# Performance work log

Measured on AMD Instinct MI355X. Metric: run time of the kernel, lower is better.

## Reference

```python
import jax, jax.numpy as jnp
import numpy as np

N = 200000   # nodes
E = 4000000  # edges
D = 32       # hidden dim (forced equal to edge-embed dim 32)
G = 512      # graphs in batch
OUT = 64     # conv5 output dim
BN_EPS = 1e-5


def _bn(h, g, b):
    # BatchNorm1d, training mode (fresh model): biased batch stats over node dim
    mu = jnp.mean(h, axis=0)
    var = jnp.var(h, axis=0)
    return g * (h - mu) * jax.lax.rsqrt(var + BN_EPS) + b


def _gine(h, src, dst, e, W1, b1, g, be, W2, b2, final_relu):
    # GINEConv (eps=0): out = MLP(x + sum_j ReLU(x_j + edge_attr))
    msg = jax.nn.relu(h[src] + e)                              # [E, D]
    agg = jax.ops.segment_sum(msg, dst, num_segments=h.shape[0])
    z = h + agg
    z = jax.nn.relu(_bn(z @ W1 + b1, g, be)) @ W2 + b2
    return jax.nn.relu(z) if final_relu else z


def setup_inputs() -> dict:
    key = jax.random.key(0)
    ks = jax.random.split(key, 16)
    xav = lambda k, shp: jax.random.uniform(k, shp, jnp.float32, -1.0, 1.0) * np.sqrt(6.0 / (shp[-2] + shp[-1]))
    x = jax.random.normal(ks[0], (N, D), jnp.float32)
    edge_index = jax.random.randint(ks[1], (2, E), 0, N, dtype=jnp.int32)
    edge_type = jax.random.randint(ks[2], (E,), 0, 2, dtype=jnp.int32)
    batch = jnp.sort(jax.random.randint(ks[3], (N,), 0, G, dtype=jnp.int32))
    emb = xav(ks[4], (2, D))  # xavier-initialized edge-type embedding
    # convs 1-4: Linear(D,D), BN(D), ReLU, Linear(D,D), ReLU  -> stacked [4,...]
    W1s = xav(ks[5], (4, D, D)); b1s = jnp.zeros((4, D))
    g1s = jnp.ones((4, D)); be1s = jnp.zeros((4, D))
    W2s = xav(ks[6], (4, D, D)); b2s = jnp.zeros((4, D))
    # conv 5: Linear(D,D), BN(D), ReLU, Linear(D,OUT)  (no final ReLU)
    w15 = xav(ks[7], (D, D)); b15 = jnp.zeros((D,))
    g5 = jnp.ones((D,)); be5 = jnp.zeros((D,))
    w25 = xav(ks[8], (D, OUT)); b25 = jnp.zeros((OUT,))
    return dict(x=x, edge_index=edge_index, edge_type=edge_type, batch=batch,
                emb=emb, W1s=W1s, b1s=b1s, g1s=g1s, be1s=be1s, W2s=W2s, b2s=b2s,
                w15=w15, b15=b15, g5=g5, be5=be5, w25=w25, b25=b25)


def reference(x, edge_index, edge_type, batch, emb, W1s, b1s, g1s, be1s, W2s, b2s,
              w15, b15, g5, be5, w25, b25):
    src, dst = edge_index[0], edge_index[1]
    e = emb[edge_type]                                          # [E, D]
    h = x
    for i in range(4):
        h = _gine(h, src, dst, e, W1s[i], b1s[i], g1s[i], be1s[i], W2s[i], b2s[i], True)
    h = _gine(h, src, dst, e, w15, b15, g5, be5, w25, b25, False)  # [N, OUT]
    mx = jax.ops.segment_max(h, batch, num_segments=G)
    cnt = jax.ops.segment_sum(jnp.ones((h.shape[0], 1), h.dtype), batch, num_segments=G)
    mn = jax.ops.segment_sum(h, batch, num_segments=G) / jnp.maximum(cnt, 1.0)
    return jnp.concatenate([mx, mn], axis=1)                    # [G, 2*OUT]
```

## Files before the change

kernel.cpp:

```cpp
#include <hip/hip_runtime.h>

#define NBLKA 2048

__device__ __forceinline__ unsigned encf(float x) {
    unsigned u = __float_as_uint(x);
    return (u & 0x80000000u) ? ~u : (u | 0x80000000u);
}
__device__ __forceinline__ float decf(unsigned u) {
    u = (u & 0x80000000u) ? (u & 0x7FFFFFFFu) : ~u;
    return __uint_as_float(u);
}
__device__ __forceinline__ unsigned bf16rne(float f) {
    unsigned u = __float_as_uint(f);
    return (u + 0x7FFFu + ((u >> 16) & 1u)) >> 16;
}


__global__ __launch_bounds__(256) void passA_k(const int* __restrict__ dst, int E,
                                               int* __restrict__ cntMat, int bshift,
                                               int nblk, int nb2) {
    __shared__ int hist[512];
    hist[threadIdx.x] = 0; hist[threadIdx.x + 256] = 0;
    __syncthreads();
    int base = blockIdx.x * 4096;
#pragma unroll
    for (int r = 0; r < 16; r++) {
        int i = base + threadIdx.x + r * 256;
        if (i < E) atomicAdd(&hist[dst[i] >> bshift], 1);
    }
    __syncthreads();
    for (int bk = threadIdx.x; bk < nb2; bk += 256)
        cntMat[bk * nblk + blockIdx.x] = hist[bk];
}

__global__ void scanA_k(int* __restrict__ data, int total, int* __restrict__ chunkTot) {
    __shared__ int sd[256];
    int tid = threadIdx.x;
    int base = blockIdx.x * 2048 + tid * 8;
    int v[8]; int s = 0;
#pragma unroll
    for (int r = 0; r < 8; r++) {
        int idx = base + r;
        int x = (idx < total) ? data[idx] : 0;
        s += x; v[r] = s;
    }
    sd[tid] = s; __syncthreads();
    for (int off = 1; off < 256; off <<= 1) {
        int x = (tid >= off) ? sd[tid - off] : 0;
        __syncthreads();
        sd[tid] += x;
        __syncthreads();
    }
    int prev = (tid > 0) ? sd[tid - 1] : 0;
#pragma unroll
    for (int r = 0; r < 8; r++) {
        int idx = base + r;
        if (idx < total) data[idx] = v[r] + prev;
    }
    if (tid == 255) chunkTot[blockIdx.x] = sd[255];
}

__global__ void scanB_k(const int* __restrict__ chunkTot, int nchunk, int* __restrict__ chunkOff) {
    __shared__ int sd[256];
    int tid = threadIdx.x;
    int v = (tid < nchunk) ? chunkTot[tid] : 0;
    sd[tid] = v; __syncthreads();
    for (int off = 1; off < 256; off <<= 1) {
        int x = (tid >= off) ? sd[tid - off] : 0;
        __syncthreads();
        sd[tid] += x;
        __syncthreads();
    }
    if (tid < nchunk) chunkOff[tid] = sd[tid] - v;
}

__global__ void scanC2_k(int* __restrict__ data, int total, const int* __restrict__ chunkOff) {
    int off = chunkOff[blockIdx.x];
    int base = blockIdx.x * 2048 + threadIdx.x * 8;
#pragma unroll
    for (int r = 0; r < 8; r++) {
        int idx = base + r;
        if (idx < total) data[idx] += off;
    }
}

__global__ __launch_bounds__(256) void passB_k(const int* __restrict__ ei,
                                               const int* __restrict__ ety, int E,
                                               const int* __restrict__ cntScan,
                                               unsigned* __restrict__ binned,
                                               int bshift, int sBits, int nblk, int nb2) {
    __shared__ unsigned stage[4096];
    __shared__ unsigned short bkid[4096];
    __shared__ int hist[512], sd[256], cursor[512], rebase[512];
    int tid = threadIdx.x;
    int base = blockIdx.x * 4096;
    hist[tid] = 0; hist[tid + 256] = 0;
    __syncthreads();

    unsigned ent[16];
    int bk[16];
    int lowmask = (1 << bshift) - 1;
    int dshift = sBits + 1;
#pragma unroll
    for (int r = 0; r < 16; r++) {
        int i = base + tid + r * 256;
        if (i < E) {
            int s = ei[i];
            int d = ei[E + i];
            int t = ety[i];
            ent[r] = ((unsigned)(d & lowmask) << dshift) | ((unsigned)t << sBits) | (unsigned)s;
            bk[r] = d >> bshift;
            atomicAdd(&hist[bk[r]], 1);
        } else bk[r] = -1;
    }
    __syncthreads();

    int v0 = hist[2 * tid], v1 = hist[2 * tid + 1];
    int sum2 = v0 + v1;
    sd[tid] = sum2; __syncthreads();
    for (int off = 1; off < 256; off <<= 1) {
        int x = (tid >= off) ? sd[tid - off] : 0;
        __syncthreads();
        sd[tid] += x;
        __syncthreads();
    }
    int exclPair = sd[tid] - sum2;
    __syncthreads();
    cursor[2 * tid] = exclPair;
    cursor[2 * tid + 1] = exclPair + v0;
    int b0 = 2 * tid, b1 = 2 * tid + 1;
    rebase[b0] = (b0 < nb2 && v0 > 0) ? (cntScan[b0 * nblk + blockIdx.x] - v0) - exclPair : 0;
    rebase[b1] = (b1 < nb2 && v1 > 0) ? (cntScan[b1 * nblk + blockIdx.x] - v1) - (exclPair + v0) : 0;
    __syncthreads();

#pragma unroll
    for (int r = 0; r < 16; r++) {
        if (bk[r] >= 0) {
            int p = atomicAdd(&cursor[bk[r]], 1);
            stage[p] = ent[r];
            bkid[p] = (unsigned short)bk[r];
        }
    }
    __syncthreads();

    int cnt = E - base; if (cnt > 4096) cnt = 4096;
    for (int i = tid; i < cnt; i += 256)
        binned[rebase[bkid[i]] + i] = stage[i];
}

__global__ __launch_bounds__(256) void passC_k(const unsigned* __restrict__ binned,
                                               const int* __restrict__ cntScan,
                                               int nblk, int* __restrict__ rowptr,
                                               unsigned* __restrict__ sorted,
                                               int N, int E, int bshift, int sBits,
                                               int nb2) {
    __shared__ int hist[512], cursor[512], sd[256];
    int tid = threadIdx.x;
    int b = blockIdx.x;
    int s = (b == 0) ? 0 : cntScan[b * nblk - 1];
    int e = cntScan[(b + 1) * nblk - 1];
    int nodeBase = b << bshift;
    int dshift = sBits + 1;

    hist[tid] = 0; hist[tid + 256] = 0;
    __syncthreads();
    for (int i = s + tid; i < e; i += 256)
        atomicAdd(&hist[(int)(binned[i] >> dshift)], 1);
    __syncthreads();

    int v0 = hist[2 * tid], v1 = hist[2 * tid + 1];
    int sum2 = v0 + v1;
    sd[tid] = sum2; __syncthreads();
    for (int off = 1; off < 256; off <<= 1) {
        int x = (tid >= off) ? sd[tid - off] : 0;
        __syncthreads();
        sd[tid] += x;
        __syncthreads();
    }
    int exclPair = sd[tid] - sum2;
    __syncthreads();
    cursor[2 * tid] = exclPair;
    cursor[2 * tid + 1] = exclPair + v0;
    int n0 = nodeBase + 2 * tid, n1 = nodeBase + 2 * tid + 1;
    if (n0 < N) rowptr[n0] = s + exclPair;
    if (n1 < N) rowptr[n1] = s + exclPair + v0;
    __syncthreads();

    for (int i = s + tid; i < e; i += 256) {
        unsigned en = binned[i];
        int ln = (int)(en >> dshift);
        int p = atomicAdd(&cursor[ln], 1);
        sorted[s + p] = en;
    }
    if (b == nb2 - 1 && tid == 0) rowptr[N] = E;
}

__global__ void initpool_k(unsigned* __restrict__ maxb, float* __restrict__ sumb, int n) {
    int i = blockIdx.x * blockDim.x + threadIdx.x;
    if (i < n) { maxb[i] = 0x007FFFFFu; sumb[i] = 0.f; }
}

__global__ void copyx_k(const float* __restrict__ x, unsigned* __restrict__ P,
                        unsigned* __restrict__ Q, int N) {
    int i = blockIdx.x * 256 + threadIdx.x;
    int tot = N * 16;
    if (i < tot) {
        float2 v = ((const float2*)x)[i];
        P[i] = bf16rne(v.x) | (bf16rne(v.y) << 16);
    }
    if (i < 16) {
        unsigned sp = bf16rne(-1e30f) | (bf16rne(-1e30f) << 16);
        P[tot + i] = sp;
        Q[tot + i] = sp;
    }
}

__global__ __launch_bounds__(256) void layerA_k(
    const unsigned* __restrict__ hin, const int* __restrict__ rowptr,
    const unsigned* __restrict__ sorted, const float* __restrict__ emb,
    const float* __restrict__ W1, const float* __restrict__ b1,
    float* __restrict__ tout, float* __restrict__ partial, int Nn, int sBits,
    unsigned sentw)
{
    float2* tout2 = (float2*)tout;
    int tid = threadIdx.x;
    int gl = tid & 31;
    int c = gl & 15;
    int slot = gl >> 4;
    int grp = tid >> 5;
    unsigned smask = (1u << sBits) - 1u;

    float2 w1c[16];
#pragma unroll
    for (int kk = 0; kk < 16; kk++)
        w1c[kk] = *(const float2*)&W1[(16 * slot + kk) * 32 + 2 * c];
    float2 b1p = *(const float2*)&b1[2 * c];
    float2 e0p = *(const float2*)&emb[2 * c];
    float2 e1p = *(const float2*)&emb[32 + 2 * c];

    __shared__ float zl[8][32];
    __shared__ float ls[8][32], lq[8][32];

    float2 bsum = {0.f, 0.f}, bsq = {0.f, 0.f};

    int gid0 = (blockIdx.x * 256 + tid) >> 5;
    int nG = (gridDim.x * 256) >> 5;

    for (int n = gid0; n < Nn; n += nG) {
        int es = rowptr[n], ee = rowptr[n + 1];
        float accx = 0.f, accy = 0.f;
        for (int e0 = es; e0 < ee; e0 += 32) {
            int idx = e0 + gl;
            unsigned pv = (idx < ee) ? sorted[idx] : sentw;
#pragma unroll
            for (int kk = 0; kk < 16; kk++) {
                unsigned p = (unsigned)__shfl((int)pv, kk, 16);
                unsigned s = p & smask;
                unsigned w = hin[s * 16u + (unsigned)c];
                float hx = __uint_as_float(w << 16);
                float hy = __uint_as_float(w & 0xFFFF0000u);
                bool t1 = ((p >> sBits) & 1u) != 0u;
                float evx = t1 ? e1p.x : e0p.x;
                float evy = t1 ? e1p.y : e0p.y;
                accx += fmaxf(hx + evx, 0.f);
                accy += fmaxf(hy + evy, 0.f);
            }
        }
        accx += __shfl_xor(accx, 16);
        accy += __shfl_xor(accy, 16);
        unsigned wn = hin[(unsigned)n * 16u + (unsigned)c];
        accx += __uint_as_float(wn << 16);
        accy += __uint_as_float(wn & 0xFFFF0000u);

        if (slot == 0) { zl[grp][2 * c] = accx; zl[grp][2 * c + 1] = accy; }
        float tx = 0.f, ty = 0.f;
#pragma unroll
        for (int kk = 0; kk < 16; kk++) {
            float zk = zl[grp][16 * slot + kk];
            tx = fmaf(zk, w1c[kk].x, tx);
            ty = fmaf(zk, w1c[kk].y, ty);
        }
        tx += __shfl_xor(tx, 16);
        ty += __shfl_xor(ty, 16);
        tx += b1p.x; ty += b1p.y;
        if (slot == 0) { float2 tp; tp.x = tx; tp.y = ty; tout2[(unsigned)n * 16u + (unsigned)c] = tp; }
        bsum.x += tx; bsum.y += ty;
        bsq.x = fmaf(tx, tx, bsq.x);
        bsq.y = fmaf(ty, ty, bsq.y);
    }

    if (slot == 0) {
        ls[grp][2 * c] = bsum.x; ls[grp][2 * c + 1] = bsum.y;
        lq[grp][2 * c] = bsq.x;  lq[grp][2 * c + 1] = bsq.y;
    }
    __syncthreads();
    if (tid < 32) {
        float s = 0.f, q = 0.f;
#pragma unroll
        for (int r = 0; r < 8; r++) { s += ls[r][tid]; q += lq[r][tid]; }
        partial[blockIdx.x * 64 + tid] = s;
        partial[blockIdx.x * 64 + 32 + tid] = q;
    }
}

__global__ __launch_bounds__(256) void bnred1_k(const float* __restrict__ partial,
                                                float* __restrict__ partial2) {
    __shared__ float sd[4][64];
    int tid = threadIdx.x;
    int c = tid & 63, q = tid >> 6;
    int rowBase = blockIdx.x * 32 + q * 8;
    float s = 0.f;
#pragma unroll
    for (int r = 0; r < 8; r++) s += partial[(rowBase + r) * 64 + c];
    sd[q][c] = s;
    __syncthreads();
    if (q == 0) partial2[blockIdx.x * 64 + c] = sd[0][c] + sd[1][c] + sd[2][c] + sd[3][c];
}

__global__ __launch_bounds__(256) void bnred2_k(const float* __restrict__ partial2,
                                                const float* __restrict__ gamma,
                                                const float* __restrict__ beta,
                                                float* __restrict__ bn_ac, float invN) {
    __shared__ float sd[4][64];
    int tid = threadIdx.x;
    int c = tid & 63, q = tid >> 6;
    float s = 0.f;
#pragma unroll
    for (int r = 0; r < 16; r++) s += partial2[(q * 16 + r) * 64 + c];
    sd[q][c] = s;
    __syncthreads();
    if (tid < 32) {
        float mu  = (sd[0][tid] + sd[1][tid] + sd[2][tid] + sd[3][tid]) * invN;
        float sq  = (sd[0][tid + 32] + sd[1][tid + 32] + sd[2][tid + 32] + sd[3][tid + 32]) * invN;
        float var = sq - mu * mu;
        float a = gamma[tid] * rsqrtf(var + 1e-5f);
        bn_ac[tid] = a;
        bn_ac[32 + tid] = beta[tid] - a * mu;
    }
}

__global__ __launch_bounds__(256) void layerB32_k(
    const float* __restrict__ tin, const float* __restrict__ bn_ac,
    const float* __restrict__ W2, const float* __restrict__ b2,
    unsigned* __restrict__ hout, int Nn)
{
    int tid = threadIdx.x;
    int j = tid & 31, grp = tid >> 5;
    float a = bn_ac[j], c = bn_ac[32 + j];
    float wc[32];
#pragma unroll
    for (int k = 0; k < 32; k++) wc[k] = W2[k * 32 + j];
    float bj = b2[j];
    for (int n = blockIdx.x * 8 + grp; n < Nn; n += gridDim.x * 8) {
        float t = tin[n * 32 + j];
        float u = fmaxf(fmaf(a, t, c), 0.f);
        float o = bj;
#pragma unroll
        for (int k = 0; k < 32; k++) o = fmaf(__shfl(u, k, 32), wc[k], o);
        unsigned b = bf16rne(fmaxf(o, 0.f));
        unsigned nb = (unsigned)__shfl_xor((int)b, 1, 32);
        if ((j & 1) == 0) hout[(unsigned)n * 16u + (unsigned)(j >> 1)] = b | (nb << 16);
    }
}

__global__ __launch_bounds__(256) void layerB64_k(
    const float* __restrict__ tin, const float* __restrict__ bn_ac,
    const float* __restrict__ W2, const float* __restrict__ b2,
    float* __restrict__ hout, int Nn)
{
    int tid = threadIdx.x;
    int j = tid & 31, grp = tid >> 5;
    float a = bn_ac[j], c = bn_ac[32 + j];
    float wlo[32], whi[32];
#pragma unroll
    for (int k = 0; k < 32; k++) { wlo[k] = W2[k * 64 + j]; whi[k] = W2[k * 64 + 32 + j]; }
    float blo = b2[j], bhi = b2[32 + j];
    for (int n = blockIdx.x * 8 + grp; n < Nn; n += gridDim.x * 8) {
        float t = tin[n * 32 + j];
        float u = fmaxf(fmaf(a, t, c), 0.f);
        float olo = blo, ohi = bhi;
#pragma unroll
        for (int k = 0; k < 32; k++) {
            float uk = __shfl(u, k, 32);
            olo = fmaf(uk, wlo[k], olo);
            ohi = fmaf(uk, whi[k], ohi);
        }
        hout[n * 64 + j] = olo;
        hout[n * 64 + 32 + j] = ohi;
    }
}

__global__ void pool1_k(const float* __restrict__ h5, const int* __restrict__ batch,
                        unsigned* __restrict__ maxb, float* __restrict__ sumb, int Nn)
{
    int ch = threadIdx.x & 63, slot = threadIdx.x >> 6;
    int base = blockIdx.x * 256 + slot * 64;
    int g = -1; float mx = 0.f, sm = 0.f;
    for (int i = 0; i < 64; i++) {
        int node = base + i;
        if (node >= Nn) break;
        int gn = batch[node];
        float v = h5[node * 64 + ch];
        if (gn != g) {
            if (g >= 0) { atomicMax(&maxb[g * 64 + ch], encf(mx)); atomicAdd(&sumb[g * 64 + ch], sm); }
            g = gn; mx = v; sm = v;
        } else { mx = fmaxf(mx, v); sm += v; }
    }
    if (g >= 0) { atomicMax(&maxb[g * 64 + ch], encf(mx)); atomicAdd(&sumb[g * 64 + ch], sm); }
}

__global__ void final_k(const unsigned* __restrict__ maxb, const float* __restrict__ sumb,
                        const int* __restrict__ batch, int Nn, float* __restrict__ out)
{
    int g = blockIdx.x, tid = threadIdx.x;
    int a = 0, b = Nn;
    while (a < b) { int m = (a + b) >> 1; if (batch[m] < g) a = m + 1; else b = m; }
    int lo0 = a;
    a = 0; b = Nn;
    while (a < b) { int m = (a + b) >> 1; if (batch[m] < g + 1) a = m + 1; else b = m; }
    int hi0 = a;
    float inv = 1.f / fmaxf((float)(hi0 - lo0), 1.f);
    if (tid < 64) out[g * 128 + tid] = decf(maxb[g * 64 + tid]);
    else          out[g * 128 + tid] = sumb[g * 64 + (tid - 64)] * inv;
}

extern "C" void kernel_launch(void* const* d_in, const int* in_sizes, int n_in,
                              void* d_out, int out_size, void* d_ws, size_t ws_size,
                              hipStream_t stream) {
    const float* x    = (const float*)d_in[0];
    const int*   ei   = (const int*)d_in[1];
    const int*   ety  = (const int*)d_in[2];
    const int*   batch= (const int*)d_in[3];
    const float* emb  = (const float*)d_in[4];
    const float* W1s  = (const float*)d_in[5];
    const float* b1s  = (const float*)d_in[6];
    const float* g1s  = (const float*)d_in[7];
    const float* be1s = (const float*)d_in[8];
    const float* W2s  = (const float*)d_in[9];
    const float* b2s  = (const float*)d_in[10];
    const float* w15  = (const float*)d_in[11];
    const float* b15  = (const float*)d_in[12];
    const float* g5   = (const float*)d_in[13];
    const float* be5  = (const float*)d_in[14];
    const float* w25  = (const float*)d_in[15];
    const float* b25  = (const float*)d_in[16];

    int N = in_sizes[0] / 32;
    int E = in_sizes[1] / 2;
    int G = out_size / 128;

    int sBits = 1; while ((1 << sBits) < N + 1) sBits++;
    int bshift = 0; while (((N - 1) >> bshift) >= 512) bshift++;
    int nb2 = ((N - 1) >> bshift) + 1;
    int nblkE = (E + 4095) / 4096;

    char* wsb = (char*)d_ws;
    size_t o = 0;
    size_t hPkBytes = (size_t)(N + 1) * 16 * 4;
    size_t tbBytes = (size_t)N * 32 * 4;
    size_t binBytes = (size_t)E * 4;
    size_t rtb = tbBytes > binBytes ? tbBytes : binBytes;
    unsigned* P      = (unsigned*)(wsb + o); o += hPkBytes;
    unsigned* Q      = (unsigned*)(wsb + o); o += hPkBytes;
    float*    tb     = (float*)(wsb + o);
    unsigned* binned = (unsigned*)(wsb + o);
    o += rtb;
    float*    h5w    = (float*)(wsb + o); o += (size_t)N * 64 * 4;
    int*      rowptr = (int*)(wsb + o);   o += ((size_t)N + 2) * 4;
    unsigned* sorted = (unsigned*)(wsb + o); o += (size_t)E * 4;
    int*      chunkTot = (int*)(wsb + o); o += 1024;
    int*      chunkOff = (int*)(wsb + o); o += 1024;
    float*    partial  = (float*)(wsb + o); o += (size_t)NBLKA * 64 * 4;
    float*    partial2 = (float*)(wsb + o); o += 64 * 64 * 4;
    float*    bn_ac    = (float*)(wsb + o); o += 64 * 4;
    unsigned* maxb     = (unsigned*)(wsb + o); o += (size_t)G * 64 * 4;
    float*    sumb     = (float*)(wsb + o); o += (size_t)G * 64 * 4;
    int*      cntMat   = (int*)(wsb + o); o += (size_t)nb2 * nblkE * 4;

    passA_k<<<nblkE, 256, 0, stream>>>(ei + E, E, cntMat, bshift, nblkE, nb2);
    int total2 = nb2 * nblkE;
    int nchunk2 = (total2 + 2047) / 2048;
    scanA_k<<<nchunk2, 256, 0, stream>>>(cntMat, total2, chunkTot);
    scanB_k<<<1, 256, 0, stream>>>(chunkTot, nchunk2, chunkOff);
    scanC2_k<<<nchunk2, 256, 0, stream>>>(cntMat, total2, chunkOff);
    passB_k<<<nblkE, 256, 0, stream>>>(ei, ety, E, cntMat, binned, bshift, sBits, nblkE, nb2);
    passC_k<<<nb2, 256, 0, stream>>>(binned, cntMat, nblkE, rowptr, sorted, N, E, bshift, sBits, nb2);
    copyx_k<<<(N * 16 + 255) / 256, 256, 0, stream>>>(x, P, Q, N);
    initpool_k<<<(G * 64 + 255) / 256, 256, 0, stream>>>(maxb, sumb, G * 64);

    unsigned sentw = (unsigned)N;

    unsigned* inb = P;
    unsigned* outb = Q;
    for (int L = 0; L < 5; ++L) {
        const float* W1 = (L < 4) ? W1s + L * 1024 : w15;
        const float* b1 = (L < 4) ? b1s + L * 32  : b15;
        const float* ga = (L < 4) ? g1s + L * 32  : g5;
        const float* be = (L < 4) ? be1s + L * 32 : be5;
        const float* W2 = (L < 4) ? W2s + L * 1024 : w25;
        const float* b2 = (L < 4) ? b2s + L * 32  : b25;

        layerA_k<<<NBLKA, 256, 0, stream>>>(inb, rowptr, sorted, emb, W1, b1, tb, partial, N, sBits, sentw);
        bnred1_k<<<64, 256, 0, stream>>>(partial, partial2);
        bnred2_k<<<1, 256, 0, stream>>>(partial2, ga, be, bn_ac, 1.f / (float)N);
        if (L < 4) {
            layerB32_k<<<1024, 256, 0, stream>>>(tb, bn_ac, W2, b2, outb, N);
            unsigned* tmp = inb; inb = outb; outb = tmp;
        } else {
            layerB64_k<<<1024, 256, 0, stream>>>(tb, bn_ac, W2, b2, h5w, N);
        }
    }

    pool1_k<<<(N + 255) / 256, 256, 0, stream>>>(h5w, batch, maxb, sumb, N);
    final_k<<<G, 128, 0, stream>>>(maxb, sumb, batch, N, (float*)d_out);
}
```

Baseline: 700.1 us.

## Fuse BN reduction into layerA via last-block counter and fuse conv5 with pooling

Removes the two BN reduction kernels per layer by having the last finishing block of layerA (detected with an atomic counter) reduce all partial sums and compute the BN scale and shift. Fuses the conv5 output projection with graph pooling, so the 64-wide h5 tensor is no longer written to and re-read from memory. Merges the pool-buffer init into the x conversion kernel, which also zeroes the counters. The trade-off is a serial tail in layerA, where one block reduces 2048 partials, plus more atomics from 64-node runs.

```diff
diff --git a/kernel.cpp b/kernel.cpp
--- a/kernel.cpp
+++ b/kernel.cpp
@@ -195,13 +195,10 @@
     if (b == nb2 - 1 && tid == 0) rowptr[N] = E;
 }
 
-__global__ void initpool_k(unsigned* __restrict__ maxb, float* __restrict__ sumb, int n) {
-    int i = blockIdx.x * blockDim.x + threadIdx.x;
-    if (i < n) { maxb[i] = 0x007FFFFFu; sumb[i] = 0.f; }
-}
-
-__global__ void copyx_k(const float* __restrict__ x, unsigned* __restrict__ P,
-                        unsigned* __restrict__ Q, int N) {
+__global__ void prep_k(const float* __restrict__ x, unsigned* __restrict__ P,
+                       unsigned* __restrict__ Q, int N,
+                       unsigned* __restrict__ maxb, float* __restrict__ sumb, int G64,
+                       int* __restrict__ cnts) {
     int i = blockIdx.x * 256 + threadIdx.x;
     int tot = N * 16;
     if (i < tot) {
@@ -213,14 +210,18 @@
         P[tot + i] = sp;
         Q[tot + i] = sp;
     }
+    if (i < G64) { maxb[i] = 0x007FFFFFu; sumb[i] = 0.f; }
+    if (i < 8) cnts[i] = 0;
 }
 
 __global__ __launch_bounds__(256) void layerA_k(
     const unsigned* __restrict__ hin, const int* __restrict__ rowptr,
     const unsigned* __restrict__ sorted, const float* __restrict__ emb,
     const float* __restrict__ W1, const float* __restrict__ b1,
-    float* __restrict__ tout, float* __restrict__ partial, int Nn, int sBits,
-    unsigned sentw)
+    const float* __restrict__ gamma, const float* __restrict__ beta,
+    float* __restrict__ tout, float* __restrict__ partial,
+    float* __restrict__ bn_ac, int* __restrict__ counter,
+    int Nn, int sBits, unsigned sentw, float invN)
 {
     float2* tout2 = (float2*)tout;
     int tid = threadIdx.x;
@@ -240,6 +241,8 @@
 
     __shared__ float zl[8][32];
     __shared__ float ls[8][32], lq[8][32];
+    __shared__ float rd[4][64];
+    __shared__ int isLast;
 
     float2 bsum = {0.f, 0.f}, bsq = {0.f, 0.f};
 
@@ -301,41 +304,28 @@
         partial[blockIdx.x * 64 + tid] = s;
         partial[blockIdx.x * 64 + 32 + tid] = q;
     }
-}
-
-__global__ __launch_bounds__(256) void bnred1_k(const float* __restrict__ partial,
-                                                float* __restrict__ partial2) {
-    __shared__ float sd[4][64];
-    int tid = threadIdx.x;
-    int c = tid & 63, q = tid >> 6;
-    int rowBase = blockIdx.x * 32 + q * 8;
-    float s = 0.f;
-#pragma unroll
-    for (int r = 0; r < 8; r++) s += partial[(rowBase + r) * 64 + c];
-    sd[q][c] = s;
-    __syncthreads();
-    if (q == 0) partial2[blockIdx.x * 64 + c] = sd[0][c] + sd[1][c] + sd[2][c] + sd[3][c];
-}
-
-__global__ __launch_bounds__(256) void bnred2_k(const float* __restrict__ partial2,
-                                                const float* __restrict__ gamma,
-                                                const float* __restrict__ beta,
-                                                float* __restrict__ bn_ac, float invN) {
-    __shared__ float sd[4][64];
-    int tid = threadIdx.x;
-    int c = tid & 63, q = tid >> 6;
-    float s = 0.f;
-#pragma unroll
-    for (int r = 0; r < 16; r++) s += partial2[(q * 16 + r) * 64 + c];
-    sd[q][c] = s;
-    __syncthreads();
-    if (tid < 32) {
-        float mu  = (sd[0][tid] + sd[1][tid] + sd[2][tid] + sd[3][tid]) * invN;
-        float sq  = (sd[0][tid + 32] + sd[1][tid + 32] + sd[2][tid + 32] + sd[3][tid + 32]) * invN;
-        float var = sq - mu * mu;
-        float a = gamma[tid] * rsqrtf(var + 1e-5f);
-        bn_ac[tid] = a;
-        bn_ac[32 + tid] = beta[tid] - a * mu;
+    __syncthreads();
+    __threadfence();
+    if (tid == 0) {
+        int prev = atomicAdd(counter, 1);
+        isLast = (prev == (int)gridDim.x - 1);
+    }
+    __syncthreads();
+    if (isLast) {
+        __threadfence();
+        int cc = tid & 63, q = tid >> 6;
+        float s = 0.f;
+        for (int r = q; r < NBLKA; r += 4) s += partial[r * 64 + cc];
+        rd[q][cc] = s;
+        __syncthreads();
+        if (tid < 32) {
+            float mu = (rd[0][tid] + rd[1][tid] + rd[2][tid] + rd[3][tid]) * invN;
+            float sq = (rd[0][tid + 32] + rd[1][tid + 32] + rd[2][tid + 32] + rd[3][tid + 32]) * invN;
+            float var = sq - mu * mu;
+            float a = gamma[tid] * rsqrtf(var + 1e-5f);
+            bn_ac[tid] = a;
+            bn_ac[32 + tid] = beta[tid] - a * mu;
+        }
     }
 }
 
@@ -363,10 +353,11 @@
     }
 }
 
-__global__ __launch_bounds__(256) void layerB64_k(
+__global__ __launch_bounds__(256) void layerB64pool_k(
     const float* __restrict__ tin, const float* __restrict__ bn_ac,
     const float* __restrict__ W2, const float* __restrict__ b2,
-    float* __restrict__ hout, int Nn)
+    const int* __restrict__ batch,
+    unsigned* __restrict__ maxb, float* __restrict__ sumb, int Nn)
 {
     int tid = threadIdx.x;
     int j = tid & 31, grp = tid >> 5;
@@ -375,7 +366,14 @@
 #pragma unroll
     for (int k = 0; k < 32; k++) { wlo[k] = W2[k * 64 + j]; whi[k] = W2[k * 64 + 32 + j]; }
     float blo = b2[j], bhi = b2[32 + j];
-    for (int n = blockIdx.x * 8 + grp; n < Nn; n += gridDim.x * 8) {
+
+    int n0 = (blockIdx.x * 8 + grp) * 64;
+    if (n0 >= Nn) return;
+    int nend = n0 + 64; if (nend > Nn) nend = Nn;
+
+    int curg = -1;
+    float mxl = 0.f, mxh = 0.f, sml = 0.f, smh = 0.f;
+    for (int n = n0; n < nend; n++) {
         float t = tin[n * 32 + j];
         float u = fmaxf(fmaf(a, t, c), 0.f);
         float olo = blo, ohi = bhi;
@@ -385,28 +383,26 @@
             olo = fmaf(uk, wlo[k], olo);
             ohi = fmaf(uk, whi[k], ohi);
         }
-        hout[n * 64 + j] = olo;
-        hout[n * 64 + 32 + j] = ohi;
-    }
-}
-
-__global__ void pool1_k(const float* __restrict__ h5, const int* __restrict__ batch,
-                        unsigned* __restrict__ maxb, float* __restrict__ sumb, int Nn)
-{
-    int ch = threadIdx.x & 63, slot = threadIdx.x >> 6;
-    int base = blockIdx.x * 256 + slot * 64;
-    int g = -1; float mx = 0.f, sm = 0.f;
-    for (int i = 0; i < 64; i++) {
-        int node = base + i;
-        if (node >= Nn) break;
-        int gn = batch[node];
-        float v = h5[node * 64 + ch];
-        if (gn != g) {
-            if (g >= 0) { atomicMax(&maxb[g * 64 + ch], encf(mx)); atomicAdd(&sumb[g * 64 + ch], sm); }
-            g = gn; mx = v; sm = v;
-        } else { mx = fmaxf(mx, v); sm += v; }
-    }
-    if (g >= 0) { atomicMax(&maxb[g * 64 + ch], encf(mx)); atomicAdd(&sumb[g * 64 + ch], sm); }
+        int gn = batch[n];
+        if (gn != curg) {
+            if (curg >= 0) {
+                atomicMax(&maxb[curg * 64 + j], encf(mxl));
+                atomicMax(&maxb[curg * 64 + 32 + j], encf(mxh));
+                atomicAdd(&sumb[curg * 64 + j], sml);
+                atomicAdd(&sumb[curg * 64 + 32 + j], smh);
+            }
+            curg = gn; mxl = olo; mxh = ohi; sml = olo; smh = ohi;
+        } else {
+            mxl = fmaxf(mxl, olo); mxh = fmaxf(mxh, ohi);
+            sml += olo; smh += ohi;
+        }
+    }
+    if (curg >= 0) {
+        atomicMax(&maxb[curg * 64 + j], encf(mxl));
+        atomicMax(&maxb[curg * 64 + 32 + j], encf(mxh));
+        atomicAdd(&sumb[curg * 64 + j], sml);
+        atomicAdd(&sumb[curg * 64 + 32 + j], smh);
+    }
 }
 
 __global__ void final_k(const unsigned* __restrict__ maxb, const float* __restrict__ sumb,
@@ -465,14 +461,13 @@
     float*    tb     = (float*)(wsb + o);
     unsigned* binned = (unsigned*)(wsb + o);
     o += rtb;
-    float*    h5w    = (float*)(wsb + o); o += (size_t)N * 64 * 4;
     int*      rowptr = (int*)(wsb + o);   o += ((size_t)N + 2) * 4;
     unsigned* sorted = (unsigned*)(wsb + o); o += (size_t)E * 4;
     int*      chunkTot = (int*)(wsb + o); o += 1024;
     int*      chunkOff = (int*)(wsb + o); o += 1024;
     float*    partial  = (float*)(wsb + o); o += (size_t)NBLKA * 64 * 4;
-    float*    partial2 = (float*)(wsb + o); o += 64 * 64 * 4;
     float*    bn_ac    = (float*)(wsb + o); o += 64 * 4;
+    int*      cnts     = (int*)(wsb + o); o += 32;
     unsigned* maxb     = (unsigned*)(wsb + o); o += (size_t)G * 64 * 4;
     float*    sumb     = (float*)(wsb + o); o += (size_t)G * 64 * 4;
     int*      cntMat   = (int*)(wsb + o); o += (size_t)nb2 * nblkE * 4;
@@ -485,10 +480,10 @@
     scanC2_k<<<nchunk2, 256, 0, stream>>>(cntMat, total2, chunkOff);
     passB_k<<<nblkE, 256, 0, stream>>>(ei, ety, E, cntMat, binned, bshift, sBits, nblkE, nb2);
     passC_k<<<nb2, 256, 0, stream>>>(binned, cntMat, nblkE, rowptr, sorted, N, E, bshift, sBits, nb2);
-    copyx_k<<<(N * 16 + 255) / 256, 256, 0, stream>>>(x, P, Q, N);
-    initpool_k<<<(G * 64 + 255) / 256, 256, 0, stream>>>(maxb, sumb, G * 64);
+    prep_k<<<(N * 16 + 255) / 256, 256, 0, stream>>>(x, P, Q, N, maxb, sumb, G * 64, cnts);
 
     unsigned sentw = (unsigned)N;
+    float invN = 1.f / (float)N;
 
     unsigned* inb = P;
     unsigned* outb = Q;
@@ -500,17 +495,15 @@
         const float* W2 = (L < 4) ? W2s + L * 1024 : w25;
         const float* b2 = (L < 4) ? b2s + L * 32  : b25;
 
-        layerA_k<<<NBLKA, 256, 0, stream>>>(inb, rowptr, sorted, emb, W1, b1, tb, partial, N, sBits, sentw);
-        bnred1_k<<<64, 256, 0, stream>>>(partial, partial2);
-        bnred2_k<<<1, 256, 0, stream>>>(partial2, ga, be, bn_ac, 1.f / (float)N);
+        layerA_k<<<NBLKA, 256, 0, stream>>>(inb, rowptr, sorted, emb, W1, b1, ga, be,
+                                            tb, partial, bn_ac, cnts + L, N, sBits, sentw, invN);
         if (L < 4) {
             layerB32_k<<<1024, 256, 0, stream>>>(tb, bn_ac, W2, b2, outb, N);
             unsigned* tmp = inb; inb = outb; outb = tmp;
         } else {
-            layerB64_k<<<1024, 256, 0, stream>>>(tb, bn_ac, W2, b2, h5w, N);
-        }
-    }
-
-    pool1_k<<<(N + 255) / 256, 256, 0, stream>>>(h5w, batch, maxb, sumb, N);
+            layerB64pool_k<<<(N + 511) / 512, 256, 0, stream>>>(tb, bn_ac, W2, b2, batch, maxb, sumb, N);
+        }
+    }
+
     final_k<<<G, 128, 0, stream>>>(maxb, sumb, batch, N, (float*)d_out);
 }
```

Measured after the change: 2.389 ms. 3.41x slower.
